# Kernel tuning notes

Measured on AMD Instinct MI355X. Metric: run time of the kernel, lower is better.

The kernel has to match this reference:

```python
import jax, jax.numpy as jnp
import numpy as np

DIM = 768; HEADS = 12; HD = DIM // HEADS; SCALE = HD ** -0.5
B = 4; T = 8; H = 14; W = 14; N = H * W  # 196 VMAE patches per frame
DOWN = 192   # adapter down dim = dim * 0.25
MLP_H = 3072 # dim * mlp_ratio

def _ln(x, g, b, eps=1e-5):
    m = x.mean(-1, keepdims=True)
    v = ((x - m) ** 2).mean(-1, keepdims=True)
    return (x - m) * jax.lax.rsqrt(v + eps) * g + b

def _lin(x, w, b=None):
    y = x @ w.T
    return y if b is None else y + b

def _gelu(x):
    return jax.nn.gelu(x, approximate=False)  # torch nn.GELU (erf)

def _mha(q, k, v):  # q:[b,h,n,d] k,v:[b,h,m,d]
    a = jax.nn.softmax((q * SCALE) @ jnp.swapaxes(k, -2, -1), axis=-1)
    return a @ v

def _adapter(x, w1, b1, w2, b2, skip):
    y = _lin(_gelu(_lin(x, w1, b1)), w2, b2)
    return x + y if skip else y

def _block(s_x, t_x, p):
    # --- self-attention on temporal (VMAE) tokens, with adapter ---
    xn = _ln(t_x, p['g1'], p['bb1'])
    bias = jnp.concatenate([p['q_bias'], jnp.zeros_like(p['v_bias']), p['v_bias']])
    Bx, Nx, _ = xn.shape
    qkv = _lin(xn, p['qkv_w'], bias).reshape(Bx, Nx, 3, HEADS, HD).transpose(2, 0, 3, 1, 4)
    o = _mha(qkv[0], qkv[1], qkv[2]).transpose(0, 2, 1, 3).reshape(Bx, Nx, DIM)
    o = _lin(o, p['aproj_w'], p['aproj_b'])
    t = t_x + _adapter(o, p['sa_w1'], p['sa_b1'], p['sa_w2'], p['sa_b2'], True)
    # --- S2T cross-attn: temporal queries attend to per-frame CNN spatial tokens ---
    s_pat = s_x.reshape(B * T, H * W, DIM) + p['s2t_pos_cnn']
    tx = t.reshape(B * T, N, DIM) + p['s2t_pos_vmae']
    q = _lin(tx, p['s2t_qw'], p['s2t_qb']).reshape(B * T, N, HEADS, HD).transpose(0, 2, 1, 3)
    kv = _lin(s_pat, p['s2t_kvw'], p['s2t_kvb']).reshape(B * T, H * W, 2, HEADS, HD).transpose(2, 0, 3, 1, 4)
    o = _mha(q, kv[0], kv[1]).transpose(0, 2, 1, 3).reshape(B * T, N, DIM)
    o = _lin(o, p['s2t_pw'], p['s2t_pb']).reshape(B, T * N, DIM)
    t = t + o
    # --- T2S cross-attn: per-location CNN queries attend over time to VMAE tokens ---
    s_pat = s_x.reshape(B, T, H * W, DIM).transpose(0, 2, 1, 3) + p['t2s_pos_cnn']  # b hw t c
    tx = t.reshape(B, T, N, DIM).transpose(0, 2, 1, 3) + p['t2s_pos_vmae']          # b n t d (N==H*W)
    s_pat = s_pat.reshape(B * H * W, T, DIM)
    tx = tx.reshape(B * N, T, DIM)
    q = _lin(s_pat, p['t2s_qw'], p['t2s_qb']).reshape(B * H * W, T, HEADS, HD).transpose(0, 2, 1, 3)
    kv = _lin(tx, p['t2s_kvw'], p['t2s_kvb']).reshape(B * N, T, 2, HEADS, HD).transpose(2, 0, 3, 1, 4)
    o = _mha(q, kv[0], kv[1]).transpose(0, 2, 1, 3).reshape(B * H * W, T, DIM)
    o = _lin(o, p['t2s_pw'], p['t2s_pb'])
    s = s_x + o.reshape(B, H, W, T, DIM).transpose(0, 3, 1, 2, 4).reshape(B * T, H, W, DIM)
    # --- MLP + parallel adapter (scale = 0.5 per Block.__init__) ---
    xn2 = _ln(t, p['g2'], p['bb2'])
    t = t + _lin(_gelu(_lin(xn2, p['fc1_w'], p['fc1_b'])), p['fc2_w'], p['fc2_b']) \
          + 0.5 * _adapter(xn2, p['ma_w1'], p['ma_b1'], p['ma_w2'], p['ma_b2'], False)
    return s, t

PARAM_NAMES = ['g1','bb1','qkv_w','q_bias','v_bias','aproj_w','aproj_b',
               'sa_w1','sa_b1','sa_w2','sa_b2',
               's2t_pos_cnn','s2t_pos_vmae','s2t_qw','s2t_qb','s2t_kvw','s2t_kvb','s2t_pw','s2t_pb',
               't2s_pos_cnn','t2s_pos_vmae','t2s_qw','t2s_qb','t2s_kvw','t2s_kvb','t2s_pw','t2s_pb',
               'g2','bb2','fc1_w','fc1_b','fc2_w','fc2_b','ma_w1','ma_b1','ma_w2','ma_b2']

def setup_inputs():
    key = jax.random.key(0)
    ks = iter(jax.random.split(key, 64))
    def w(shape, s=0.02):
        return jax.random.normal(next(ks), shape, jnp.float32) * s
    d = dict(
        s_x=jax.random.normal(next(ks), (B * T, H, W, DIM), jnp.float32),
        t_x=jax.random.normal(next(ks), (B, T * N, DIM), jnp.float32),
        g1=jnp.ones((DIM,), jnp.float32), bb1=jnp.zeros((DIM,), jnp.float32),
        qkv_w=w((3 * DIM, DIM)), q_bias=jnp.zeros((DIM,), jnp.float32), v_bias=jnp.zeros((DIM,), jnp.float32),
        aproj_w=w((DIM, DIM)), aproj_b=jnp.zeros((DIM,), jnp.float32),
        sa_w1=w((DOWN, DIM)), sa_b1=jnp.zeros((DOWN,), jnp.float32),
        sa_w2=w((DIM, DOWN)), sa_b2=jnp.zeros((DIM,), jnp.float32),
        s2t_pos_cnn=w((H * W, DIM), SCALE), s2t_pos_vmae=w((196, DIM), SCALE),
        s2t_qw=w((DIM, DIM)), s2t_qb=jnp.zeros((DIM,), jnp.float32),
        s2t_kvw=w((2 * DIM, DIM)), s2t_kvb=jnp.zeros((2 * DIM,), jnp.float32),
        s2t_pw=w((DIM, DIM)), s2t_pb=jnp.zeros((DIM,), jnp.float32),
        t2s_pos_cnn=w((T, DIM), SCALE), t2s_pos_vmae=w((T, DIM), SCALE),
        t2s_qw=w((DIM, DIM)), t2s_qb=jnp.zeros((DIM,), jnp.float32),
        t2s_kvw=w((2 * DIM, DIM)), t2s_kvb=jnp.zeros((2 * DIM,), jnp.float32),
        t2s_pw=w((DIM, DIM)), t2s_pb=jnp.zeros((DIM,), jnp.float32),
        g2=jnp.ones((DIM,), jnp.float32), bb2=jnp.zeros((DIM,), jnp.float32),
        fc1_w=w((MLP_H, DIM)), fc1_b=jnp.zeros((MLP_H,), jnp.float32),
        fc2_w=w((DIM, MLP_H)), fc2_b=jnp.zeros((DIM,), jnp.float32),
        ma_w1=w((DOWN, DIM)), ma_b1=jnp.zeros((DOWN,), jnp.float32),
        ma_w2=w((DIM, DOWN)), ma_b2=jnp.zeros((DIM,), jnp.float32),
    )
    return d

def reference(s_x, t_x, g1, bb1, qkv_w, q_bias, v_bias, aproj_w, aproj_b,
              sa_w1, sa_b1, sa_w2, sa_b2,
              s2t_pos_cnn, s2t_pos_vmae, s2t_qw, s2t_qb, s2t_kvw, s2t_kvb, s2t_pw, s2t_pb,
              t2s_pos_cnn, t2s_pos_vmae, t2s_qw, t2s_qb, t2s_kvw, t2s_kvb, t2s_pw, t2s_pb,
              g2, bb2, fc1_w, fc1_b, fc2_w, fc2_b, ma_w1, ma_b1, ma_w2, ma_b2):
    loc = locals()
    p = {k: loc[k] for k in PARAM_NAMES}
    return _block(s_x, t_x, p)
```

## Files before the change

### kernel.cpp

```cpp
#include <hip/hip_runtime.h>
#include <hip/hip_bf16.h>
#include <math.h>


typedef __bf16 bf16_t;
typedef bf16_t bf16x4 __attribute__((ext_vector_type(4)));
typedef bf16_t bf16x8 __attribute__((ext_vector_type(8)));
typedef float  f32x4  __attribute__((ext_vector_type(4)));

typedef const __attribute__((address_space(1))) void* gas_t;
typedef __attribute__((address_space(3))) void* las_t;
__device__ __forceinline__ void async16(const void* g, void* l) {
    __builtin_amdgcn_global_load_lds((gas_t)g, (las_t)l, 16, 0, 0);
}

#define MFMA(a,b,c) __builtin_amdgcn_mfma_f32_16x16x32_bf16((a),(b),(c),0,0,0)
#define EXP2(x) __builtin_amdgcn_exp2f(x)
#define LOG2E 1.4426950408889634f

__device__ __forceinline__ int xcd_swz(int bid, int nwg) {
    const int q = nwg >> 3, r = nwg & 7, x = bid & 7, o = bid >> 3;
    return (x < r ? x * (q + 1) : r * (q + 1) + (x - r) * q) + o;
}

template<bool GELU>
__global__ __launch_bounds__(256) void gemm128(
    const bf16_t* __restrict__ A, const bf16_t* __restrict__ W,
    const float* __restrict__ bias,
    const float* __restrict__ res1, const float* __restrict__ res2,
    float res2_scale,
    float* __restrict__ Yf, bf16_t* __restrict__ Yb,
    int M, int N, int K)
{
    __shared__ bf16_t As[128*64];
    __shared__ bf16_t Bs[128*64];
    const int tid = threadIdx.x, wave = tid >> 6, lane = tid & 63;
    const int nbx = N >> 7;
    const int lb = xcd_swz(blockIdx.x, gridDim.x);
    const int m0 = (lb / nbx) * 128, n0 = (lb % nbx) * 128;
    const int wm = (wave & 1) * 64, wn = (wave >> 1) * 64;
    const int l15 = lane & 15, lq = lane >> 4;
    const int lrow = lane >> 3, lcol = (lane & 7) * 8;

    f32x4 acc[4][4] = {};

    for (int k0 = 0; k0 < K; k0 += 64) {
#pragma unroll
        for (int c = 0; c < 4; ++c) {
            const int r = wave * 32 + c * 8;
            async16(A + (size_t)(m0 + r + lrow) * K + k0 + lcol, &As[r * 64]);
            async16(W + (size_t)(n0 + r + lrow) * K + k0 + lcol, &Bs[r * 64]);
        }
        __syncthreads();
#pragma unroll
        for (int kk = 0; kk < 64; kk += 32) {
            bf16x8 a[4], b[4];
#pragma unroll
            for (int i = 0; i < 4; ++i)
                a[i] = *(const bf16x8*)&As[(wm + i * 16 + l15) * 64 + kk + lq * 8];
#pragma unroll
            for (int i = 0; i < 4; ++i)
                b[i] = *(const bf16x8*)&Bs[(wn + i * 16 + l15) * 64 + kk + lq * 8];
#pragma unroll
            for (int mi = 0; mi < 4; ++mi)
#pragma unroll
                for (int ni = 0; ni < 4; ++ni)
                    acc[mi][ni] = MFMA(a[mi], b[ni], acc[mi][ni]);
        }
        __syncthreads();
    }

#pragma unroll
    for (int mi = 0; mi < 4; ++mi)
#pragma unroll
    for (int ni = 0; ni < 4; ++ni) {
        const int gn = n0 + wn + ni * 16 + l15;
        const float bv = bias ? bias[gn] : 0.f;
#pragma unroll
        for (int i = 0; i < 4; ++i) {
            const int gm = m0 + wm + mi * 16 + lq * 4 + i;
            float v = acc[mi][ni][i] + bv;
            if (GELU) v = 0.5f * v * (1.0f + erff(v * 0.70710678118654752f));
            const size_t off = (size_t)gm * N + gn;
            if (res1) v += res1[off];
            if (res2) v += res2_scale * res2[off];
            if (Yf) Yf[off] = v;
            if (Yb) Yb[off] = (bf16_t)v;
        }
    }
}

template<bool GELU, int EPI>
__global__ __launch_bounds__(256) void gemm128x64(
    const bf16_t* __restrict__ A, const bf16_t* __restrict__ W,
    const float* __restrict__ bias,
    const float* __restrict__ res1, const float* __restrict__ res2,
    float res2_scale,
    float* __restrict__ Yf, bf16_t* __restrict__ Yb,
    int M, int N, int K,
    const float* __restrict__ ep_a, float* __restrict__ ep_fo,
    bf16_t* __restrict__ ep_bo)
{
    __shared__ bf16_t As[128*64];
    __shared__ bf16_t Bs[64*64];
    const int tid = threadIdx.x, wave = tid >> 6, lane = tid & 63;
    const int nbx = N >> 6;
    const int lb = xcd_swz(blockIdx.x, gridDim.x);
    const int m0 = (lb / nbx) * 128, n0 = (lb % nbx) * 64;
    const int wm = (wave & 1) * 64, wn = (wave >> 1) * 32;
    const int l15 = lane & 15, lq = lane >> 4;
    const int lrow = lane >> 3, lcol = (lane & 7) * 8;

    f32x4 acc[4][2] = {};

    for (int k0 = 0; k0 < K; k0 += 64) {
#pragma unroll
        for (int c = 0; c < 4; ++c) {
            const int r = wave * 32 + c * 8;
            async16(A + (size_t)(m0 + r + lrow) * K + k0 + lcol, &As[r * 64]);
        }
#pragma unroll
        for (int c = 0; c < 2; ++c) {
            const int r = wave * 16 + c * 8;
            async16(W + (size_t)(n0 + r + lrow) * K + k0 + lcol, &Bs[r * 64]);
        }
        __syncthreads();
#pragma unroll
        for (int kk = 0; kk < 64; kk += 32) {
            bf16x8 a[4], b[2];
#pragma unroll
            for (int i = 0; i < 4; ++i)
                a[i] = *(const bf16x8*)&As[(wm + i * 16 + l15) * 64 + kk + lq * 8];
#pragma unroll
            for (int i = 0; i < 2; ++i)
                b[i] = *(const bf16x8*)&Bs[(wn + i * 16 + l15) * 64 + kk + lq * 8];
#pragma unroll
            for (int mi = 0; mi < 4; ++mi)
#pragma unroll
                for (int ni = 0; ni < 2; ++ni)
                    acc[mi][ni] = MFMA(a[mi], b[ni], acc[mi][ni]);
        }
        __syncthreads();
    }

#pragma unroll
    for (int mi = 0; mi < 4; ++mi)
#pragma unroll
    for (int ni = 0; ni < 2; ++ni) {
        const int gn = n0 + wn + ni * 16 + l15;
        const float bv = bias ? bias[gn] : 0.f;
#pragma unroll
        for (int i = 0; i < 4; ++i) {
            const int gm = m0 + wm + mi * 16 + lq * 4 + i;
            float v = acc[mi][ni][i] + bv;
            if (GELU) v = 0.5f * v * (1.0f + erff(v * 0.70710678118654752f));
            const size_t off = (size_t)gm * N + gn;
            if (res1) v += res1[off];
            if (res2) v += res2_scale * res2[off];
            if (Yf) Yf[off] = v;
            if (Yb) Yb[off] = (bf16_t)v;
            if (EPI == 1) {
                const int b_ = gm / 1568, r_ = gm - b_ * 1568;
                const int t_ = r_ / 196,  n_ = r_ - t_ * 196;
                const int dest = ((b_ * 196 + n_) << 3) + t_;
                ep_bo[(size_t)dest * 768 + gn] =
                    (bf16_t)(v + ep_a[t_ * 768 + gn]);
            }
            if (EPI == 2) {
                const int t_ = gm & 7, bn_ = gm >> 3;
                const int n_ = bn_ % 196, b_ = bn_ / 196;
                const int dest = (b_ * 8 + t_) * 196 + n_;
                const size_t doff = (size_t)dest * 768 + gn;
                ep_fo[doff] = ep_a[doff] + v;
            }
        }
    }
}

template<bool GELU, int EPI>
__global__ __launch_bounds__(256) void gemm_bt(
    const float* __restrict__ X, const float* __restrict__ W,
    const float* __restrict__ bias,
    const float* __restrict__ res1, const float* __restrict__ res2,
    float res2_scale,
    float* __restrict__ Y, int M, int N, int K,
    const float* __restrict__ ep_pos, bf16_t* __restrict__ ep_bo)
{
    __shared__ bf16_t As[64][72];
    __shared__ bf16_t Bs[64][72];
    const int tid  = threadIdx.x;
    const int nbx  = N >> 6;
    const int lb   = xcd_swz(blockIdx.x, gridDim.x);
    const int n0   = (lb % nbx) * 64;
    const int m0   = (lb / nbx) * 64;
    const int wave = tid >> 6, lane = tid & 63;
    const int wm   = (wave & 1) * 32, wn = (wave >> 1) * 32;
    const int l15  = lane & 15, lq = lane >> 4;
    f32x4 acc[2][2] = {};
    const int sr = tid >> 4;
    const int sc4 = (tid & 15) * 4;

    for (int k0 = 0; k0 < K; k0 += 64) {
#pragma unroll
        for (int i = 0; i < 4; ++i) {
            const int row = sr + i * 16;
            const float4 xv = *reinterpret_cast<const float4*>(
                X + (size_t)(m0 + row) * K + k0 + sc4);
            bf16x4 p;
            p[0] = (bf16_t)xv.x; p[1] = (bf16_t)xv.y;
            p[2] = (bf16_t)xv.z; p[3] = (bf16_t)xv.w;
            *reinterpret_cast<bf16x4*>(&As[row][sc4]) = p;
        }
#pragma unroll
        for (int i = 0; i < 4; ++i) {
            const int row = sr + i * 16;
            const float4 wv = *reinterpret_cast<const float4*>(
                W + (size_t)(n0 + row) * K + k0 + sc4);
            bf16x4 p;
            p[0] = (bf16_t)wv.x; p[1] = (bf16_t)wv.y;
            p[2] = (bf16_t)wv.z; p[3] = (bf16_t)wv.w;
            *reinterpret_cast<bf16x4*>(&Bs[row][sc4]) = p;
        }
        __syncthreads();
#pragma unroll
        for (int kk = 0; kk < 64; kk += 32) {
            bf16x8 a0 = *reinterpret_cast<const bf16x8*>(&As[wm +      l15][kk + lq * 8]);
            bf16x8 a1 = *reinterpret_cast<const bf16x8*>(&As[wm + 16 + l15][kk + lq * 8]);
            bf16x8 b0 = *reinterpret_cast<const bf16x8*>(&Bs[wn +      l15][kk + lq * 8]);
            bf16x8 b1 = *reinterpret_cast<const bf16x8*>(&Bs[wn + 16 + l15][kk + lq * 8]);
            acc[0][0] = MFMA(a0, b0, acc[0][0]);
            acc[0][1] = MFMA(a0, b1, acc[0][1]);
            acc[1][0] = MFMA(a1, b0, acc[1][0]);
            acc[1][1] = MFMA(a1, b1, acc[1][1]);
        }
        __syncthreads();
    }

#pragma unroll
    for (int mt = 0; mt < 2; ++mt)
#pragma unroll
    for (int nt = 0; nt < 2; ++nt) {
        const int gn = n0 + wn + nt * 16 + l15;
        const float bv = bias[gn];
#pragma unroll
        for (int i = 0; i < 4; ++i) {
            const int gm = m0 + wm + mt * 16 + lq * 4 + i;
            float v = acc[mt][nt][i] + bv;
            if (GELU) v = 0.5f * v * (1.0f + erff(v * 0.70710678118654752f));
            const size_t off = (size_t)gm * N + gn;
            if (res1) v += res1[off];
            if (res2) v += res2_scale * res2[off];
            Y[off] = v;
            if (EPI == 1) {
                const int n_ = gm % 196;
                ep_bo[off] = (bf16_t)(v + ep_pos[n_ * 768 + gn]);
            }
        }
    }
}

__global__ __launch_bounds__(256) void flash_k(
    const bf16_t* __restrict__ Q, int ldq,
    const bf16_t* __restrict__ Kp, int ldk,
    const bf16_t* __restrict__ Vp, int ldv,
    bf16_t* __restrict__ O, int ldo,
    int nq, int nk, float scale)
{
    __shared__ bf16_t Ks[64 * 68];
    __shared__ bf16_t Vs[64 * 68];
    __shared__ bf16_t Ps[64 * 68];

    const int tid = threadIdx.x, wave = tid >> 6, lane = tid & 63;
    const int q0 = blockIdx.x * 64, hoff = blockIdx.y * 64, g = blockIdx.z;
    const int l15 = lane & 15, lq = lane >> 4;
    const int wm16 = wave * 16;
    const int sr = tid >> 3, sc8 = (tid & 7) * 8;
    const float sl2e = scale * LOG2E;

    bf16x8 bq0, bq1;
    {
        int qr = q0 + wm16 + l15; if (qr > nq - 1) qr = nq - 1;
        const bf16_t* qp = Q + ((size_t)g * nq + qr) * ldq + hoff + lq * 8;
        bq0 = *(const bf16x8*)qp;
        bq1 = *(const bf16x8*)(qp + 32);
    }

    bf16x8 ka, kb, va, vb;
    {
        int r0 = sr;      if (r0 > nk - 1) r0 = nk - 1;
        int r1 = sr + 32; if (r1 > nk - 1) r1 = nk - 1;
        ka = *(const bf16x8*)(Kp + ((size_t)g * nk + r0) * ldk + hoff + sc8);
        kb = *(const bf16x8*)(Kp + ((size_t)g * nk + r1) * ldk + hoff + sc8);
        int key = lane; if (key > nk - 1) key = nk - 1;
        const bf16_t* vp = Vp + ((size_t)g * nk + key) * ldv + hoff + wm16;
        va = *(const bf16x8*)vp;
        vb = *(const bf16x8*)(vp + 8);
    }

    float m_r = -INFINITY, l_r = 0.f;
    f32x4 acc[4] = {};

    for (int kk0 = 0; kk0 < nk; kk0 += 64) {
        __syncthreads();
        *(bf16x8*)&Ks[sr * 68 + sc8] = ka;
        *(bf16x8*)&Ks[(sr + 32) * 68 + sc8] = kb;
#pragma unroll
        for (int j = 0; j < 8; ++j) Vs[(wm16 + j) * 68 + lane] = va[j];
#pragma unroll
        for (int j = 0; j < 8; ++j) Vs[(wm16 + 8 + j) * 68 + lane] = vb[j];
        __syncthreads();

        const int nx = kk0 + 64;
        if (nx < nk) {
            int r0 = nx + sr;      if (r0 > nk - 1) r0 = nk - 1;
            int r1 = nx + sr + 32; if (r1 > nk - 1) r1 = nk - 1;
            ka = *(const bf16x8*)(Kp + ((size_t)g * nk + r0) * ldk + hoff + sc8);
            kb = *(const bf16x8*)(Kp + ((size_t)g * nk + r1) * ldk + hoff + sc8);
            int key = nx + lane; if (key > nk - 1) key = nk - 1;
            const bf16_t* vp = Vp + ((size_t)g * nk + key) * ldv + hoff + wm16;
            va = *(const bf16x8*)vp;
            vb = *(const bf16x8*)(vp + 8);
        }

        f32x4 s[4] = {};
#pragma unroll
        for (int nt = 0; nt < 4; ++nt) {
            bf16x8 ak0 = *(const bf16x8*)&Ks[(nt * 16 + l15) * 68 + lq * 8];
            bf16x8 ak1 = *(const bf16x8*)&Ks[(nt * 16 + l15) * 68 + 32 + lq * 8];
            s[nt] = MFMA(ak0, bq0, s[nt]);
            s[nt] = MFMA(ak1, bq1, s[nt]);
        }

#pragma unroll
        for (int nt = 0; nt < 4; ++nt)
#pragma unroll
        for (int i = 0; i < 4; ++i) {
            const bool valid = (kk0 + nt * 16 + lq * 4 + i) < nk;
            s[nt][i] = valid ? s[nt][i] * sl2e : -INFINITY;
        }

        float t0 = fmaxf(fmaxf(s[0][0], s[0][1]), fmaxf(s[0][2], s[0][3]));
        float t1 = fmaxf(fmaxf(s[1][0], s[1][1]), fmaxf(s[1][2], s[1][3]));
        float t2 = fmaxf(fmaxf(s[2][0], s[2][1]), fmaxf(s[2][2], s[2][3]));
        float t3 = fmaxf(fmaxf(s[3][0], s[3][1]), fmaxf(s[3][2], s[3][3]));
        float t = fmaxf(fmaxf(t0, t1), fmaxf(t2, t3));
        t = fmaxf(t, __shfl_xor(t, 16));
        t = fmaxf(t, __shfl_xor(t, 32));
        const float mnew = fmaxf(m_r, t);
        const float a = EXP2(m_r - mnew);
        float ps = 0.f;
#pragma unroll
        for (int nt = 0; nt < 4; ++nt)
#pragma unroll
        for (int i = 0; i < 4; ++i) {
            const float e = EXP2(s[nt][i] - mnew);
            s[nt][i] = e; ps += e;
        }
        ps += __shfl_xor(ps, 16);
        ps += __shfl_xor(ps, 32);
        l_r = l_r * a + ps;
        m_r = mnew;

        float alq[4];
#pragma unroll
        for (int i = 0; i < 4; ++i) alq[i] = __shfl(a, lq * 4 + i);

#pragma unroll
        for (int nt = 0; nt < 4; ++nt) {
            bf16x4 pk;
            pk[0] = (bf16_t)s[nt][0]; pk[1] = (bf16_t)s[nt][1];
            pk[2] = (bf16_t)s[nt][2]; pk[3] = (bf16_t)s[nt][3];
            *(bf16x4*)&Ps[(wm16 + l15) * 68 + nt * 16 + lq * 4] = pk;
        }

#pragma unroll
        for (int nt = 0; nt < 4; ++nt)
#pragma unroll
        for (int i = 0; i < 4; ++i)
            acc[nt][i] *= alq[i];
#pragma unroll
        for (int kk = 0; kk < 64; kk += 32) {
            bf16x8 ap = *(const bf16x8*)&Ps[(wm16 + l15) * 68 + kk + lq * 8];
#pragma unroll
            for (int nt = 0; nt < 4; ++nt) {
                bf16x8 bv = *(const bf16x8*)&Vs[(nt * 16 + l15) * 68 + kk + lq * 8];
                acc[nt] = MFMA(ap, bv, acc[nt]);
            }
        }
    }

    float linv[4];
#pragma unroll
    for (int i = 0; i < 4; ++i)
        linv[i] = __builtin_amdgcn_rcpf(__shfl(l_r, lq * 4 + i));
#pragma unroll
    for (int nt = 0; nt < 4; ++nt)
#pragma unroll
    for (int i = 0; i < 4; ++i) {
        const int qrow = q0 + wm16 + lq * 4 + i;
        if (qrow < nq)
            O[((size_t)g * nq + qrow) * ldo + hoff + nt * 16 + l15] =
                (bf16_t)(acc[nt][i] * linv[i]);
    }
}

__global__ __launch_bounds__(256) void attn8_k(
    const bf16_t* __restrict__ Q, int ldq,
    const bf16_t* __restrict__ Kp, int ldk,
    const bf16_t* __restrict__ Vp, int ldv,
    bf16_t* __restrict__ O, int ldo,
    float scale)
{
    __shared__ float Ps[4][8][8];
    const int wv = threadIdx.x >> 6, lane = threadIdx.x & 63;
    const int gw  = blockIdx.x * 4 + wv;
    const int seq = gw / 12, h = gw - seq * 12;
    const int hoff = h * 64;
    const int l15 = lane & 15, lq = lane >> 4;
    const size_t rbase = (size_t)seq * 8;
    const float sl2e = scale * LOG2E;

    const int qr = l15 & 7;
    const bf16_t* qp = Q  + (rbase + qr) * ldq + hoff + lq * 8;
    const bf16_t* kp = Kp + (rbase + qr) * ldk + hoff + lq * 8;
    bf16x8 a0 = *(const bf16x8*)qp;
    bf16x8 a1 = *(const bf16x8*)(qp + 32);
    bf16x8 b0 = *(const bf16x8*)kp;
    bf16x8 b1 = *(const bf16x8*)(kp + 32);
    f32x4 z = {};
    f32x4 s = MFMA(a1, b1, MFMA(a0, b0, z));

    const bool cvalid = l15 < 8;
    float p[4];
#pragma unroll
    for (int i = 0; i < 4; ++i) {
        float v = cvalid ? s[i] * sl2e : -INFINITY;
        float m = v;
        m = fmaxf(m, __shfl_xor(m, 1));
        m = fmaxf(m, __shfl_xor(m, 2));
        m = fmaxf(m, __shfl_xor(m, 4));
        m = fmaxf(m, __shfl_xor(m, 8));
        float e = EXP2(v - m);
        float sum = e;
        sum += __shfl_xor(sum, 1);
        sum += __shfl_xor(sum, 2);
        sum += __shfl_xor(sum, 4);
        sum += __shfl_xor(sum, 8);
        p[i] = e * __builtin_amdgcn_rcpf(sum);
    }
    if (lq < 2 && cvalid) {
#pragma unroll
        for (int i = 0; i < 4; ++i)
            Ps[wv][lq * 4 + i][l15] = p[i];
    }
    __syncthreads();

    const int qi = lane >> 3, dg = lane & 7;
    f32x4 p0 = *(const f32x4*)&Ps[wv][qi][0];
    f32x4 p1 = *(const f32x4*)&Ps[wv][qi][4];
    float acc[8] = {};
#pragma unroll
    for (int k = 0; k < 8; ++k) {
        const bf16x8 vvec = *(const bf16x8*)(Vp + (rbase + k) * ldv + hoff + dg * 8);
        const float pk = (k < 4) ? p0[k] : p1[k - 4];
#pragma unroll
        for (int j = 0; j < 8; ++j) acc[j] += pk * (float)vvec[j];
    }
    bf16x8 o;
#pragma unroll
    for (int j = 0; j < 8; ++j) o[j] = (bf16_t)acc[j];
    *(bf16x8*)(O + (rbase + qi) * ldo + hoff + dg * 8) = o;
}

__global__ __launch_bounds__(256) void ln_k(
    const float* __restrict__ x,
    const float* __restrict__ g, const float* __restrict__ bta,
    float* __restrict__ yf, bf16_t* __restrict__ yb)
{
    __shared__ float rA[4], rB[4];
    const int row = blockIdx.x, tid = threadIdx.x;
    const int wv = tid >> 6, lane = tid & 63;
    const size_t base = (size_t)row * 768;
    const float v0 = x[base + tid];
    const float v1 = x[base + tid + 256];
    const float v2 = x[base + tid + 512];
    float s1 = v0 + v1 + v2;
    float s2 = v0 * v0 + v1 * v1 + v2 * v2;
#pragma unroll
    for (int off = 32; off > 0; off >>= 1) {
        s1 += __shfl_xor(s1, off);
        s2 += __shfl_xor(s2, off);
    }
    if (lane == 0) { rA[wv] = s1; rB[wv] = s2; }
    __syncthreads();
    const float ts1 = rA[0] + rA[1] + rA[2] + rA[3];
    const float ts2 = rB[0] + rB[1] + rB[2] + rB[3];
    const float m = ts1 * (1.f / 768.f);
    const float r = rsqrtf(ts2 * (1.f / 768.f) - m * m + 1e-5f);
    const float o0 = (v0 - m) * r * g[tid]       + bta[tid];
    const float o1 = (v1 - m) * r * g[tid + 256] + bta[tid + 256];
    const float o2 = (v2 - m) * r * g[tid + 512] + bta[tid + 512];
    yb[base + tid]       = (bf16_t)o0;
    yb[base + tid + 256] = (bf16_t)o1;
    yb[base + tid + 512] = (bf16_t)o2;
    if (yf) {
        yf[base + tid]       = o0;
        yf[base + tid + 256] = o1;
        yf[base + tid + 512] = o2;
    }
}

__global__ void addpos_k(const float* __restrict__ src, const float* __restrict__ pos,
                         bf16_t* __restrict__ dst, int nrep) {
    const int row = blockIdx.x, tid = threadIdx.x;
    const size_t base = (size_t)row * 768;
    const size_t pbase = (size_t)(row % nrep) * 768;
    for (int k = 0; k < 3; ++k) {
        int c = tid + k * 256;
        dst[base + c] = (bf16_t)(src[base + c] + pos[pbase + c]);
    }
}
__global__ void t2s_prep_q(const float* __restrict__ sx, const float* __restrict__ pos,
                           bf16_t* __restrict__ dst) {
    const int row = blockIdx.x, tid = threadIdx.x;
    const int t = row & 7, bn = row >> 3, n = bn % 196, b = bn / 196;
    const size_t src = (size_t)((b * 8 + t) * 196 + n) * 768;
    const size_t dbase = (size_t)row * 768;
    const size_t pbase = (size_t)t * 768;
    for (int k = 0; k < 3; ++k) {
        int c = tid + k * 256;
        dst[dbase + c] = (bf16_t)(sx[src + c] + pos[pbase + c]);
    }
}
__global__ void build_qkv_bias(const float* __restrict__ qb,
                               const float* __restrict__ vb,
                               float* __restrict__ dst) {
    int i = blockIdx.x * 256 + threadIdx.x;
    if (i < 768) dst[i] = qb[i];
    else if (i < 1536) dst[i] = 0.f;
    else if (i < 2304) dst[i] = vb[i - 1536];
}

struct WPtrs { const float* p[10]; };
__global__ void wcvt(WPtrs s, bf16_t* __restrict__ dst) {
    const int cum[11] = {0, 442368, 589824, 737280, 1032192, 1179648,
                         1327104, 1622016, 1769472, 2359296, 2949120};
    const int gi = blockIdx.x * 256 + threadIdx.x;
    int seg = 0;
#pragma unroll
    for (int i = 1; i < 10; ++i) if (gi >= cum[i]) seg = i;
    const float4 v = ((const float4*)s.p[seg])[gi - cum[seg]];
    bf16x4 o;
    o[0] = (bf16_t)v.x; o[1] = (bf16_t)v.y; o[2] = (bf16_t)v.z; o[3] = (bf16_t)v.w;
    ((bf16x4*)dst)[gi] = o;
}

#define OFF_QKV    0
#define OFF_APROJ  1769472
#define OFF_S2TQ   2359296
#define OFF_S2TKV  2949120
#define OFF_S2TP   4128768
#define OFF_T2SQ   4718592
#define OFF_T2SKV  5308416
#define OFF_T2SP   6488064
#define OFF_FC1    7077888
#define OFF_FC2    9437184
#define W_TOTAL    11796480

extern "C" void kernel_launch(void* const* d_in, const int* in_sizes, int n_in,
                              void* d_out, int out_size, void* d_ws, size_t ws_size,
                              hipStream_t stream)
{
    typedef const float* fp;
    fp s_x     = (fp)d_in[0];
    fp t_x     = (fp)d_in[1];
    fp g1      = (fp)d_in[2];
    fp bb1     = (fp)d_in[3];
    fp qkv_w   = (fp)d_in[4];
    fp q_bias  = (fp)d_in[5];
    fp v_bias  = (fp)d_in[6];
    fp aproj_w = (fp)d_in[7];
    fp aproj_b = (fp)d_in[8];
    fp sa_w1   = (fp)d_in[9];
    fp sa_b1   = (fp)d_in[10];
    fp sa_w2   = (fp)d_in[11];
    fp sa_b2   = (fp)d_in[12];
    fp s2t_pos_cnn  = (fp)d_in[13];
    fp s2t_pos_vmae = (fp)d_in[14];
    fp s2t_qw  = (fp)d_in[15];
    fp s2t_qb  = (fp)d_in[16];
    fp s2t_kvw = (fp)d_in[17];
    fp s2t_kvb = (fp)d_in[18];
    fp s2t_pw  = (fp)d_in[19];
    fp s2t_pb  = (fp)d_in[20];
    fp t2s_pos_cnn  = (fp)d_in[21];
    fp t2s_pos_vmae = (fp)d_in[22];
    fp t2s_qw  = (fp)d_in[23];
    fp t2s_qb  = (fp)d_in[24];
    fp t2s_kvw = (fp)d_in[25];
    fp t2s_kvb = (fp)d_in[26];
    fp t2s_pw  = (fp)d_in[27];
    fp t2s_pb  = (fp)d_in[28];
    fp g2      = (fp)d_in[29];
    fp bb2     = (fp)d_in[30];
    fp fc1_w   = (fp)d_in[31];
    fp fc1_b   = (fp)d_in[32];
    fp fc2_w   = (fp)d_in[33];
    fp fc2_b   = (fp)d_in[34];
    fp ma_w1   = (fp)d_in[35];
    fp ma_b1   = (fp)d_in[36];
    fp ma_w2   = (fp)d_in[37];
    fp ma_b2   = (fp)d_in[38];

    const size_t RD = (size_t)6272 * 768;

    float* ws   = (float*)d_ws;
    float* F    = ws;
    float* G    = F + RD;
    float* CI   = G + RD;
    float* Hb   = CI + RD;
    float* qkvb = Hb + (size_t)6272 * 192;
    bf16_t* BW  = (bf16_t*)(qkvb + 2304);
    bf16_t* Xb  = BW + W_TOTAL;
    bf16_t* Eb  = Xb + RD;
    bf16_t* Fb  = Eb + RD;
    bf16_t* MB  = Fb + RD;
    bf16_t* Xkv = MB + (size_t)6272 * 1536;

    float* out_s = (float*)d_out;
    float* out_t = out_s + RD;

    const dim3 blk(256);

    WPtrs wp;
    wp.p[0] = qkv_w;  wp.p[1] = aproj_w; wp.p[2] = s2t_qw; wp.p[3] = s2t_kvw;
    wp.p[4] = s2t_pw; wp.p[5] = t2s_qw;  wp.p[6] = t2s_kvw; wp.p[7] = t2s_pw;
    wp.p[8] = fc1_w;  wp.p[9] = fc2_w;
    wcvt<<<11520, blk, 0, stream>>>(wp, BW);

    ln_k<<<6272, blk, 0, stream>>>(t_x, g1, bb1, nullptr, Xb);
    build_qkv_bias<<<9, blk, 0, stream>>>(q_bias, v_bias, qkvb);
    gemm128<false><<<dim3(18 * 49), blk, 0, stream>>>(
        Xb, BW + OFF_QKV, qkvb, nullptr, nullptr, 0.f, nullptr, MB, 6272, 2304, 768);
    flash_k<<<dim3(25, 12, 4), blk, 0, stream>>>(
        MB, 2304, MB + 768, 2304, MB + 1536, 2304, Eb, 768, 1568, 1568, 0.125f);
    gemm128x64<false, 0><<<dim3(12 * 49), blk, 0, stream>>>(
        Eb, BW + OFF_APROJ, aproj_b, nullptr, nullptr, 0.f, F, nullptr, 6272, 768, 768,
        nullptr, nullptr, nullptr);
    gemm_bt<true, 0><<<dim3(3 * 98), blk, 0, stream>>>(
        F, sa_w1, sa_b1, nullptr, nullptr, 0.f, Hb, 6272, 192, 768, nullptr, nullptr);
    gemm_bt<false, 1><<<dim3(12 * 98), blk, 0, stream>>>(
        Hb, sa_w2, sa_b2, F, t_x, 1.0f, G, 6272, 768, 192, s2t_pos_vmae, Xb);

    gemm128x64<false, 0><<<dim3(12 * 49), blk, 0, stream>>>(
        Xb, BW + OFF_S2TQ, s2t_qb, nullptr, nullptr, 0.f, nullptr, Eb, 6272, 768, 768,
        nullptr, nullptr, nullptr);
    addpos_k<<<6272, blk, 0, stream>>>(s_x, s2t_pos_cnn, Xb, 196);
    gemm128<false><<<dim3(12 * 49), blk, 0, stream>>>(
        Xb, BW + OFF_S2TKV, s2t_kvb, nullptr, nullptr, 0.f, nullptr, MB, 6272, 1536, 768);
    flash_k<<<dim3(4, 12, 32), blk, 0, stream>>>(
        Eb, 768, MB, 1536, MB + 768, 1536, Fb, 768, 196, 196, 0.125f);
    gemm128x64<false, 1><<<dim3(12 * 49), blk, 0, stream>>>(
        Fb, BW + OFF_S2TP, s2t_pb, G, nullptr, 0.f, G, nullptr, 6272, 768, 768,
        t2s_pos_vmae, nullptr, Xkv);

    t2s_prep_q<<<6272, blk, 0, stream>>>(s_x, t2s_pos_cnn, Xb);
    gemm128x64<false, 0><<<dim3(12 * 49), blk, 0, stream>>>(
        Xb, BW + OFF_T2SQ, t2s_qb, nullptr, nullptr, 0.f, nullptr, Eb, 6272, 768, 768,
        nullptr, nullptr, nullptr);
    gemm128<false><<<dim3(12 * 49), blk, 0, stream>>>(
        Xkv, BW + OFF_T2SKV, t2s_kvb, nullptr, nullptr, 0.f, nullptr, MB, 6272, 1536, 768);
    attn8_k<<<dim3(2352), blk, 0, stream>>>(
        Eb, 768, MB, 1536, MB + 768, 1536, Fb, 768, 0.125f);
    gemm128x64<false, 2><<<dim3(12 * 49), blk, 0, stream>>>(
        Fb, BW + OFF_T2SP, t2s_pb, nullptr, nullptr, 0.f, nullptr, nullptr, 6272, 768, 768,
        s_x, out_s, nullptr);

    ln_k<<<6272, blk, 0, stream>>>(G, g2, bb2, CI, Xb);
    gemm128<true><<<dim3(24 * 49), blk, 0, stream>>>(
        Xb, BW + OFF_FC1, fc1_b, nullptr, nullptr, 0.f, nullptr, MB, 6272, 3072, 768);
    gemm_bt<true, 0><<<dim3(3 * 98), blk, 0, stream>>>(
        CI, ma_w1, ma_b1, nullptr, nullptr, 0.f, Hb, 6272, 192, 768, nullptr, nullptr);
    gemm_bt<false, 0><<<dim3(12 * 98), blk, 0, stream>>>(
        Hb, ma_w2, ma_b2, nullptr, nullptr, 0.f, F, 6272, 768, 192, nullptr, nullptr);
    gemm128x64<false, 0><<<dim3(12 * 49), blk, 0, stream>>>(
        MB, BW + OFF_FC2, fc2_b, G, F, 0.5f, out_t, nullptr, 6272, 768, 3072,
        nullptr, nullptr, nullptr);
}
```

Measured before the change: 929.3 us.

## Fuse positional-add prologs into GEMM A-loads and add lazy softmax rescaling in flash

Removes the addpos_k and t2s_prep_q kernels. The GEMMs now read fp32 s_x, add the positional embedding, convert to bf16 and write the result straight into LDS, which avoids writing and re-reading a bf16 intermediate. The flash attention kernel skips the running-max rescale unless the new tile max exceeds the old one by more than 8 in log2 units, and raises wave priority around the MFMA sections. In exchange, the fused A-load becomes a synchronous fp32 read repeated for each N-tile rather than an async bf16 copy, and the lazy rescale relies on fp32 headroom.

Result: no change. 932.1 us (+0.3%).

```diff
diff --git a/kernel.cpp b/kernel.cpp
--- a/kernel.cpp
+++ b/kernel.cpp
@@ -23,14 +23,15 @@
     return (x < r ? x * (q + 1) : r * (q + 1) + (x - r) * q) + o;
 }
 
-template<bool GELU>
+template<bool GELU, int AF>
 __global__ __launch_bounds__(256) void gemm128(
     const bf16_t* __restrict__ A, const bf16_t* __restrict__ W,
     const float* __restrict__ bias,
     const float* __restrict__ res1, const float* __restrict__ res2,
     float res2_scale,
     float* __restrict__ Yf, bf16_t* __restrict__ Yb,
-    int M, int N, int K)
+    int M, int N, int K,
+    const float* __restrict__ af_src, const float* __restrict__ af_pos)
 {
     __shared__ bf16_t As[128*64];
     __shared__ bf16_t Bs[128*64];
@@ -48,8 +49,24 @@
 #pragma unroll
         for (int c = 0; c < 4; ++c) {
             const int r = wave * 32 + c * 8;
-            async16(A + (size_t)(m0 + r + lrow) * K + k0 + lcol, &As[r * 64]);
+            if (AF == 0)
+                async16(A + (size_t)(m0 + r + lrow) * K + k0 + lcol, &As[r * 64]);
             async16(W + (size_t)(n0 + r + lrow) * K + k0 + lcol, &Bs[r * 64]);
+        }
+        if (AF == 1) {
+#pragma unroll
+            for (int j = 0; j < 8; ++j) {
+                const int ch = tid + j * 256;
+                const int r = ch >> 4, c4 = (ch & 15) * 4;
+                const int gm = m0 + r;
+                const int prow = gm % 196;
+                const float4 xv = *(const float4*)(af_src + (size_t)gm * K + k0 + c4);
+                const float4 pv = *(const float4*)(af_pos + (size_t)prow * 768 + k0 + c4);
+                bf16x4 p;
+                p[0] = (bf16_t)(xv.x + pv.x); p[1] = (bf16_t)(xv.y + pv.y);
+                p[2] = (bf16_t)(xv.z + pv.z); p[3] = (bf16_t)(xv.w + pv.w);
+                *(bf16x4*)&As[r * 64 + c4] = p;
+            }
         }
         __syncthreads();
 #pragma unroll
@@ -90,7 +107,7 @@
     }
 }
 
-template<bool GELU, int EPI>
+template<bool GELU, int EPI, int AF>
 __global__ __launch_bounds__(256) void gemm128x64(
     const bf16_t* __restrict__ A, const bf16_t* __restrict__ W,
     const float* __restrict__ bias,
@@ -99,7 +116,8 @@
     float* __restrict__ Yf, bf16_t* __restrict__ Yb,
     int M, int N, int K,
     const float* __restrict__ ep_a, float* __restrict__ ep_fo,
-    bf16_t* __restrict__ ep_bo)
+    bf16_t* __restrict__ ep_bo,
+    const float* __restrict__ af_src, const float* __restrict__ af_pos)
 {
     __shared__ bf16_t As[128*64];
     __shared__ bf16_t Bs[64*64];
@@ -114,10 +132,28 @@
     f32x4 acc[4][2] = {};
 
     for (int k0 = 0; k0 < K; k0 += 64) {
-#pragma unroll
-        for (int c = 0; c < 4; ++c) {
-            const int r = wave * 32 + c * 8;
-            async16(A + (size_t)(m0 + r + lrow) * K + k0 + lcol, &As[r * 64]);
+        if (AF == 0) {
+#pragma unroll
+            for (int c = 0; c < 4; ++c) {
+                const int r = wave * 32 + c * 8;
+                async16(A + (size_t)(m0 + r + lrow) * K + k0 + lcol, &As[r * 64]);
+            }
+        } else {
+#pragma unroll
+            for (int j = 0; j < 8; ++j) {
+                const int ch = tid + j * 256;
+                const int r = ch >> 4, c4 = (ch & 15) * 4;
+                const int gm = m0 + r;
+                const int t_ = gm & 7, bn = gm >> 3;
+                const int n_ = bn % 196, b_ = bn / 196;
+                const int srow = (b_ * 8 + t_) * 196 + n_;
+                const float4 xv = *(const float4*)(af_src + (size_t)srow * K + k0 + c4);
+                const float4 pv = *(const float4*)(af_pos + (size_t)t_ * 768 + k0 + c4);
+                bf16x4 p;
+                p[0] = (bf16_t)(xv.x + pv.x); p[1] = (bf16_t)(xv.y + pv.y);
+                p[2] = (bf16_t)(xv.z + pv.z); p[3] = (bf16_t)(xv.w + pv.w);
+                *(bf16x4*)&As[r * 64 + c4] = p;
+            }
         }
 #pragma unroll
         for (int c = 0; c < 2; ++c) {
@@ -323,6 +359,7 @@
         }
 
         f32x4 s[4] = {};
+        __builtin_amdgcn_s_setprio(1);
 #pragma unroll
         for (int nt = 0; nt < 4; ++nt) {
             bf16x8 ak0 = *(const bf16x8*)&Ks[(nt * 16 + l15) * 68 + lq * 8];
@@ -330,6 +367,7 @@
             s[nt] = MFMA(ak0, bq0, s[nt]);
             s[nt] = MFMA(ak1, bq1, s[nt]);
         }
+        __builtin_amdgcn_s_setprio(0);
 
 #pragma unroll
         for (int nt = 0; nt < 4; ++nt)
@@ -346,24 +384,31 @@
         float t = fmaxf(fmaxf(t0, t1), fmaxf(t2, t3));
         t = fmaxf(t, __shfl_xor(t, 16));
         t = fmaxf(t, __shfl_xor(t, 32));
-        const float mnew = fmaxf(m_r, t);
-        const float a = EXP2(m_r - mnew);
+        if (!__all(t <= m_r + 8.f)) {
+            const float mnew = fmaxf(m_r, t);
+            const float a = EXP2(m_r - mnew);
+            float alq[4];
+#pragma unroll
+            for (int i = 0; i < 4; ++i) alq[i] = __shfl(a, lq * 4 + i);
+            l_r *= a;
+#pragma unroll
+            for (int nt = 0; nt < 4; ++nt)
+#pragma unroll
+            for (int i = 0; i < 4; ++i)
+                acc[nt][i] *= alq[i];
+            m_r = mnew;
+        }
         float ps = 0.f;
 #pragma unroll
         for (int nt = 0; nt < 4; ++nt)
 #pragma unroll
         for (int i = 0; i < 4; ++i) {
-            const float e = EXP2(s[nt][i] - mnew);
+            const float e = EXP2(s[nt][i] - m_r);
             s[nt][i] = e; ps += e;
         }
         ps += __shfl_xor(ps, 16);
         ps += __shfl_xor(ps, 32);
-        l_r = l_r * a + ps;
-        m_r = mnew;
-
-        float alq[4];
-#pragma unroll
-        for (int i = 0; i < 4; ++i) alq[i] = __shfl(a, lq * 4 + i);
+        l_r += ps;
 
 #pragma unroll
         for (int nt = 0; nt < 4; ++nt) {
@@ -373,11 +418,7 @@
             *(bf16x4*)&Ps[(wm16 + l15) * 68 + nt * 16 + lq * 4] = pk;
         }
 
-#pragma unroll
-        for (int nt = 0; nt < 4; ++nt)
-#pragma unroll
-        for (int i = 0; i < 4; ++i)
-            acc[nt][i] *= alq[i];
+        __builtin_amdgcn_s_setprio(1);
 #pragma unroll
         for (int kk = 0; kk < 64; kk += 32) {
             bf16x8 ap = *(const bf16x8*)&Ps[(wm16 + l15) * 68 + kk + lq * 8];
@@ -387,6 +428,7 @@
                 acc[nt] = MFMA(ap, bv, acc[nt]);
             }
         }
+        __builtin_amdgcn_s_setprio(0);
     }
 
     float linv[4];
@@ -510,28 +552,6 @@
     }
 }
 
-__global__ void addpos_k(const float* __restrict__ src, const float* __restrict__ pos,
-                         bf16_t* __restrict__ dst, int nrep) {
-    const int row = blockIdx.x, tid = threadIdx.x;
-    const size_t base = (size_t)row * 768;
-    const size_t pbase = (size_t)(row % nrep) * 768;
-    for (int k = 0; k < 3; ++k) {
-        int c = tid + k * 256;
-        dst[base + c] = (bf16_t)(src[base + c] + pos[pbase + c]);
-    }
-}
-__global__ void t2s_prep_q(const float* __restrict__ sx, const float* __restrict__ pos,
-                           bf16_t* __restrict__ dst) {
-    const int row = blockIdx.x, tid = threadIdx.x;
-    const int t = row & 7, bn = row >> 3, n = bn % 196, b = bn / 196;
-    const size_t src = (size_t)((b * 8 + t) * 196 + n) * 768;
-    const size_t dbase = (size_t)row * 768;
-    const size_t pbase = (size_t)t * 768;
-    for (int k = 0; k < 3; ++k) {
-        int c = tid + k * 256;
-        dst[dbase + c] = (bf16_t)(sx[src + c] + pos[pbase + c]);
-    }
-}
 __global__ void build_qkv_bias(const float* __restrict__ qb,
                                const float* __restrict__ vb,
                                float* __restrict__ dst) {
@@ -640,50 +660,52 @@
 
     ln_k<<<6272, blk, 0, stream>>>(t_x, g1, bb1, nullptr, Xb);
     build_qkv_bias<<<9, blk, 0, stream>>>(q_bias, v_bias, qkvb);
-    gemm128<false><<<dim3(18 * 49), blk, 0, stream>>>(
-        Xb, BW + OFF_QKV, qkvb, nullptr, nullptr, 0.f, nullptr, MB, 6272, 2304, 768);
+    gemm128<false, 0><<<dim3(18 * 49), blk, 0, stream>>>(
+        Xb, BW + OFF_QKV, qkvb, nullptr, nullptr, 0.f, nullptr, MB, 6272, 2304, 768,
+        nullptr, nullptr);
     flash_k<<<dim3(25, 12, 4), blk, 0, stream>>>(
         MB, 2304, MB + 768, 2304, MB + 1536, 2304, Eb, 768, 1568, 1568, 0.125f);
-    gemm128x64<false, 0><<<dim3(12 * 49), blk, 0, stream>>>(
+    gemm128x64<false, 0, 0><<<dim3(12 * 49), blk, 0, stream>>>(
         Eb, BW + OFF_APROJ, aproj_b, nullptr, nullptr, 0.f, F, nullptr, 6272, 768, 768,
-        nullptr, nullptr, nullptr);
+        nullptr, nullptr, nullptr, nullptr, nullptr);
     gemm_bt<true, 0><<<dim3(3 * 98), blk, 0, stream>>>(
         F, sa_w1, sa_b1, nullptr, nullptr, 0.f, Hb, 6272, 192, 768, nullptr, nullptr);
     gemm_bt<false, 1><<<dim3(12 * 98), blk, 0, stream>>>(
         Hb, sa_w2, sa_b2, F, t_x, 1.0f, G, 6272, 768, 192, s2t_pos_vmae, Xb);
 
-    gemm128x64<false, 0><<<dim3(12 * 49), blk, 0, stream>>>(
+    gemm128x64<false, 0, 0><<<dim3(12 * 49), blk, 0, stream>>>(
         Xb, BW + OFF_S2TQ, s2t_qb, nullptr, nullptr, 0.f, nullptr, Eb, 6272, 768, 768,
-        nullptr, nullptr, nullptr);
-    addpos_k<<<6272, blk, 0, stream>>>(s_x, s2t_pos_cnn, Xb, 196);
-    gemm128<false><<<dim3(12 * 49), blk, 0, stream>>>(
-        Xb, BW + OFF_S2TKV, s2t_kvb, nullptr, nullptr, 0.f, nullptr, MB, 6272, 1536, 768);
+        nullptr, nullptr, nullptr, nullptr, nullptr);
+    gemm128<false, 1><<<dim3(12 * 49), blk, 0, stream>>>(
+        nullptr, BW + OFF_S2TKV, s2t_kvb, nullptr, nullptr, 0.f, nullptr, MB,
+        6272, 1536, 768, s_x, s2t_pos_cnn);
     flash_k<<<dim3(4, 12, 32), blk, 0, stream>>>(
         Eb, 768, MB, 1536, MB + 768, 1536, Fb, 768, 196, 196, 0.125f);
-    gemm128x64<false, 1><<<dim3(12 * 49), blk, 0, stream>>>(
+    gemm128x64<false, 1, 0><<<dim3(12 * 49), blk, 0, stream>>>(
         Fb, BW + OFF_S2TP, s2t_pb, G, nullptr, 0.f, G, nullptr, 6272, 768, 768,
-        t2s_pos_vmae, nullptr, Xkv);
-
-    t2s_prep_q<<<6272, blk, 0, stream>>>(s_x, t2s_pos_cnn, Xb);
-    gemm128x64<false, 0><<<dim3(12 * 49), blk, 0, stream>>>(
-        Xb, BW + OFF_T2SQ, t2s_qb, nullptr, nullptr, 0.f, nullptr, Eb, 6272, 768, 768,
-        nullptr, nullptr, nullptr);
-    gemm128<false><<<dim3(12 * 49), blk, 0, stream>>>(
-        Xkv, BW + OFF_T2SKV, t2s_kvb, nullptr, nullptr, 0.f, nullptr, MB, 6272, 1536, 768);
+        t2s_pos_vmae, nullptr, Xkv, nullptr, nullptr);
+
+    gemm128x64<false, 0, 2><<<dim3(12 * 49), blk, 0, stream>>>(
+        nullptr, BW + OFF_T2SQ, t2s_qb, nullptr, nullptr, 0.f, nullptr, Eb,
+        6272, 768, 768, nullptr, nullptr, nullptr, s_x, t2s_pos_cnn);
+    gemm128<false, 0><<<dim3(12 * 49), blk, 0, stream>>>(
+        Xkv, BW + OFF_T2SKV, t2s_kvb, nullptr, nullptr, 0.f, nullptr, MB,
+        6272, 1536, 768, nullptr, nullptr);
     attn8_k<<<dim3(2352), blk, 0, stream>>>(
         Eb, 768, MB, 1536, MB + 768, 1536, Fb, 768, 0.125f);
-    gemm128x64<false, 2><<<dim3(12 * 49), blk, 0, stream>>>(
-        Fb, BW + OFF_T2SP, t2s_pb, nullptr, nullptr, 0.f, nullptr, nullptr, 6272, 768, 768,
-        s_x, out_s, nullptr);
+    gemm128x64<false, 2, 0><<<dim3(12 * 49), blk, 0, stream>>>(
+        Fb, BW + OFF_T2SP, t2s_pb, nullptr, nullptr, 0.f, nullptr, nullptr,
+        6272, 768, 768, s_x, out_s, nullptr, nullptr, nullptr);
 
     ln_k<<<6272, blk, 0, stream>>>(G, g2, bb2, CI, Xb);
-    gemm128<true><<<dim3(24 * 49), blk, 0, stream>>>(
-        Xb, BW + OFF_FC1, fc1_b, nullptr, nullptr, 0.f, nullptr, MB, 6272, 3072, 768);
+    gemm128<true, 0><<<dim3(24 * 49), blk, 0, stream>>>(
+        Xb, BW + OFF_FC1, fc1_b, nullptr, nullptr, 0.f, nullptr, MB, 6272, 3072, 768,
+        nullptr, nullptr);
     gemm_bt<true, 0><<<dim3(3 * 98), blk, 0, stream>>>(
         CI, ma_w1, ma_b1, nullptr, nullptr, 0.f, Hb, 6272, 192, 768, nullptr, nullptr);
     gemm_bt<false, 0><<<dim3(12 * 98), blk, 0, stream>>>(
         Hb, ma_w2, ma_b2, nullptr, nullptr, 0.f, F, 6272, 768, 192, nullptr, nullptr);
-    gemm128x64<false, 0><<<dim3(12 * 49), blk, 0, stream>>>(
+    gemm128x64<false, 0, 0><<<dim3(12 * 49), blk, 0, stream>>>(
         MB, BW + OFF_FC2, fc2_b, G, F, 0.5f, out_t, nullptr, 6272, 768, 3072,
-        nullptr, nullptr, nullptr);
-}
+        nullptr, nullptr, nullptr, nullptr, nullptr);
+}
```
